# Performance work log

Hardware: AMD Instinct MI355X
Metric: run time of the kernel (lower is better)

Reference implementation:

```python
import jax, jax.numpy as jnp
import numpy as np

D_MODEL = 1024
N_HEADS = 16
D_HEAD = 64
NUM_REL_POS = 2047
B = 8
L = 1024


def setup_inputs() -> dict:
    key = jax.random.key(0)
    ks = jax.random.split(key, 8)
    s = 1.0 / np.sqrt(D_MODEL)
    x = jax.random.normal(ks[0], (B, L, D_MODEL), dtype=jnp.float32)
    rel_indices = jax.random.randint(ks[1], (L, L), 0, NUM_REL_POS)
    Wq = jax.random.normal(ks[2], (D_MODEL, D_MODEL), dtype=jnp.float32) * s
    Wk = jax.random.normal(ks[3], (D_MODEL, D_MODEL), dtype=jnp.float32) * s
    Wv = jax.random.normal(ks[4], (D_MODEL, D_MODEL), dtype=jnp.float32) * s
    Wo = jax.random.normal(ks[5], (D_MODEL, D_MODEL), dtype=jnp.float32) * s
    rel_k = jax.random.normal(ks[6], (NUM_REL_POS, D_HEAD), dtype=jnp.float32) * 0.02
    rel_v = jax.random.normal(ks[7], (NUM_REL_POS, D_HEAD), dtype=jnp.float32) * 0.02
    return {"x": x, "rel_indices": rel_indices, "Wq": Wq, "Wk": Wk,
            "Wv": Wv, "Wo": Wo, "rel_k": rel_k, "rel_v": rel_v}


def reference(x, rel_indices, Wq, Wk, Wv, Wo, rel_k, rel_v):
    Bz, Ls, D = x.shape
    H, dk = N_HEADS, D_HEAD
    scale = 1.0 / np.sqrt(dk)
    # torch Linear: y = x @ W.T, weights are [out, in]
    q = jnp.einsum('bld,ed->ble', x, Wq).reshape(Bz, Ls, H, dk).transpose(0, 2, 1, 3)
    k = jnp.einsum('bld,ed->ble', x, Wk).reshape(Bz, Ls, H, dk).transpose(0, 2, 1, 3)
    v = jnp.einsum('bld,ed->ble', x, Wv).reshape(Bz, Ls, H, dk).transpose(0, 2, 1, 3)
    r_k = rel_k[rel_indices]  # (L, L, dk)
    r_v = rel_v[rel_indices]  # (L, L, dk)
    content = jnp.einsum('bhid,bhjd->bhij', q, k)
    rel = jnp.einsum('bhid,ijd->bhij', q, r_k)
    scores = (content + rel) * scale
    probs = jax.nn.softmax(scores, axis=-1)  # dropout = 0 (eval)
    out = jnp.einsum('bhij,bhjd->bhid', probs, v) + jnp.einsum('bhij,ijd->bhid', probs, r_v)
    out = out.transpose(0, 2, 1, 3).reshape(Bz, Ls, D)
    return jnp.einsum('bld,ed->ble', out, Wo)
```

## Files before the change

kernel.cpp:

```cpp
#include <hip/hip_runtime.h>

#define B_ 8
#define H_ 16
#define L_ 1024
#define DH_ 64
#define DM_ 1024
#define NP_ 2047
#define NP2_ 2048
#define SCALE_ 0.125f

#define PS_ 1032
#define HS_ 260

typedef __attribute__((ext_vector_type(8))) short bf16x8;
typedef __attribute__((ext_vector_type(4))) float f32x4;

__device__ __forceinline__ unsigned short f2bf(float x) {
    union { float f; unsigned int u; } v; v.f = x;
    return (unsigned short)((v.u + 0x7FFFu + ((v.u >> 16) & 1u)) >> 16);
}
__device__ __forceinline__ float bf2f(unsigned short b) {
    union { unsigned int u; float f; } v; v.u = ((unsigned int)b) << 16;
    return v.f;
}

template <int MODE>
__global__ __launch_bounds__(256) void proj_gemm(const float* __restrict__ X,
                                                 const float* __restrict__ W,
                                                 float* __restrict__ Yf,
                                                 unsigned short* __restrict__ Y0,
                                                 unsigned short* __restrict__ Y1)
{
    __shared__ __align__(16) float As[16][132];
    __shared__ __align__(16) float Bs[16][132];
    const int t   = threadIdx.x;
    const int tm  = t & 15;
    const int tn  = t >> 4;
    const int row0 = blockIdx.x * 128;
    const int col0 = blockIdx.y * 128;
    const int lr  = t >> 1;
    const int lc  = (t & 1) * 8;

    float acc[8][8];
#pragma unroll
    for (int i = 0; i < 8; ++i)
#pragma unroll
        for (int j = 0; j < 8; ++j) acc[i][j] = 0.f;

    float4 xa, xb, wa, wb;
    const float* xp = X + (size_t)(row0 + lr) * DM_ + lc;
    const float* wp = W + (size_t)(col0 + lr) * DM_ + lc;
    xa = *(const float4*)(xp);     xb = *(const float4*)(xp + 4);
    wa = *(const float4*)(wp);     wb = *(const float4*)(wp + 4);

    for (int k0 = 0; k0 < DM_; k0 += 16) {
        __syncthreads();
        As[lc + 0][lr] = xa.x; As[lc + 1][lr] = xa.y; As[lc + 2][lr] = xa.z; As[lc + 3][lr] = xa.w;
        As[lc + 4][lr] = xb.x; As[lc + 5][lr] = xb.y; As[lc + 6][lr] = xb.z; As[lc + 7][lr] = xb.w;
        Bs[lc + 0][lr] = wa.x; Bs[lc + 1][lr] = wa.y; Bs[lc + 2][lr] = wa.z; Bs[lc + 3][lr] = wa.w;
        Bs[lc + 4][lr] = wb.x; Bs[lc + 5][lr] = wb.y; Bs[lc + 6][lr] = wb.z; Bs[lc + 7][lr] = wb.w;
        __syncthreads();
        if (k0 + 16 < DM_) {
            xa = *(const float4*)(xp + k0 + 16);  xb = *(const float4*)(xp + k0 + 20);
            wa = *(const float4*)(wp + k0 + 16);  wb = *(const float4*)(wp + k0 + 20);
        }
#pragma unroll
        for (int kk = 0; kk < 16; ++kk) {
            float4 a0 = *(const float4*)&As[kk][tm * 4];
            float4 a1 = *(const float4*)&As[kk][64 + tm * 4];
            float4 b0 = *(const float4*)&Bs[kk][tn * 8];
            float4 b1 = *(const float4*)&Bs[kk][tn * 8 + 4];
            const float av[8] = {a0.x, a0.y, a0.z, a0.w, a1.x, a1.y, a1.z, a1.w};
            const float bv[8] = {b0.x, b0.y, b0.z, b0.w, b1.x, b1.y, b1.z, b1.w};
#pragma unroll
            for (int i = 0; i < 8; ++i)
#pragma unroll
                for (int j = 0; j < 8; ++j)
                    acc[i][j] = fmaf(av[i], bv[j], acc[i][j]);
        }
    }

    const int bidx = row0 >> 10;
    const int hbase = blockIdx.y * 2 + (tn >> 3);
    const int dbase = (tn & 7) * 8;

    if constexpr (MODE == 1) {
#pragma unroll
        for (int i = 0; i < 8; ++i) {
            const int row = row0 + ((i < 4) ? (tm * 4 + i) : (64 + tm * 4 + i - 4));
            *(float4*)(Yf + (size_t)row * DM_ + col0 + tn * 8)     = make_float4(acc[i][0], acc[i][1], acc[i][2], acc[i][3]);
            *(float4*)(Yf + (size_t)row * DM_ + col0 + tn * 8 + 4) = make_float4(acc[i][4], acc[i][5], acc[i][6], acc[i][7]);
        }
    }
    if constexpr (MODE == 0) {
#pragma unroll
        for (int i = 0; i < 8; ++i) {
            const int row = row0 + ((i < 4) ? (tm * 4 + i) : (64 + tm * 4 + i - 4));
            const int l = row & 1023;
            const size_t base = (((size_t)bidx * H_ + hbase) * L_ + l) * DH_ + dbase;
#pragma unroll
            for (int jh = 0; jh < 2; ++jh) {
                ushort4 hi4, lo4;
                unsigned short* hp = (unsigned short*)&hi4;
                unsigned short* lp = (unsigned short*)&lo4;
#pragma unroll
                for (int j = 0; j < 4; ++j) {
                    const float y = acc[i][jh * 4 + j];
                    unsigned short hb = f2bf(y);
                    hp[j] = hb;
                    lp[j] = f2bf(y - bf2f(hb));
                }
                *(ushort4*)(Y0 + base + jh * 4) = hi4;
                *(ushort4*)(Y1 + base + jh * 4) = lo4;
            }
        }
    }
    if constexpr (MODE == 2) {
#pragma unroll
        for (int j = 0; j < 8; ++j) {
            const int d = dbase + j;
            const size_t cb = ((size_t)(bidx * H_ + hbase) * DH_ + d) * L_;
#pragma unroll
            for (int half = 0; half < 2; ++half) {
                const int l0 = (row0 & 1023) + half * 64 + tm * 4;
                ushort4 v4;
                unsigned short* vp = (unsigned short*)&v4;
#pragma unroll
                for (int i = 0; i < 4; ++i) vp[i] = f2bf(acc[half * 4 + i][j]);
                *(ushort4*)(Y0 + cb + l0) = v4;
            }
        }
    }
}

__global__ __launch_bounds__(256) void prep_rel(const float* __restrict__ rk,
                                                const float* __restrict__ rv,
                                                unsigned short* __restrict__ rk_hi,
                                                unsigned short* __restrict__ rv_t)
{
    const int idx = blockIdx.x * 256 + threadIdx.x;
    const int p = idx >> 6;
    const int d = idx & 63;
    float xk = (p < NP_) ? rk[(size_t)p * DH_ + d] : 0.f;
    rk_hi[idx] = f2bf(xk);
    float xv = (p < NP_) ? rv[(size_t)p * DH_ + d] : 0.f;
    rv_t[(size_t)d * NP2_ + p] = f2bf(xv);
}

__global__ __launch_bounds__(512, 4) void shaw_attn_mfma(
    const unsigned short* __restrict__ qh, const unsigned short* __restrict__ ql,
    const unsigned short* __restrict__ kh, const unsigned short* __restrict__ kl,
    const unsigned short* __restrict__ vt, const int* __restrict__ ridx,
    const unsigned short* __restrict__ rkh, const unsigned short* __restrict__ rvt,
    float* __restrict__ out)
{
    __shared__ __align__(16) unsigned char regionA[16 * PS_ * 2];
    __shared__ __align__(16) unsigned char regionB[16 * HS_ * 4];
    __shared__ float pmax[16][8];
    __shared__ float psum[16][8];

    char*           qrel8 = (char*)regionA;
    unsigned short* Pu    = (unsigned short*)regionA;
    float*          hist  = (float*)regionB;
    float*          red   = (float*)regionB;

    const int t    = threadIdx.x;
    const int w    = t >> 6;
    const int lane = t & 63;
    const int mrow = lane & 15;
    const int grp  = lane >> 4;
    const int i0   = blockIdx.x * 16;
    const int h    = blockIdx.y;
    const int b    = blockIdx.z;
    const size_t bh = (size_t)b * H_ + h;

    const unsigned short* qhp = qh + bh * (size_t)(L_ * DH_);
    const unsigned short* qlp = ql + bh * (size_t)(L_ * DH_);
    const unsigned short* khp = kh + bh * (size_t)(L_ * DH_);
    const unsigned short* klp = kl + bh * (size_t)(L_ * DH_);
    const unsigned short* vtp = vt + bh * (size_t)(DH_ * L_);

    bf16x8 qAh[2], qAl[2];
#pragma unroll
    for (int s = 0; s < 2; ++s) {
        const size_t off = (size_t)(i0 + mrow) * DH_ + s * 32 + grp * 8;
        qAh[s] = *(const bf16x8*)(qhp + off);
        qAl[s] = *(const bf16x8*)(qlp + off);
    }

    {
        const unsigned short* rb = rkh + (size_t)(w * 256 + mrow) * DH_ + grp * 8;
#pragma unroll 4
        for (int tt = 0; tt < 16; ++tt) {
            bf16x8 Bh0 = *(const bf16x8*)(rb + tt * 1024);
            bf16x8 Bh1 = *(const bf16x8*)(rb + tt * 1024 + 32);
            f32x4 c = {0.f, 0.f, 0.f, 0.f};
            c = __builtin_amdgcn_mfma_f32_16x16x32_bf16(qAh[0], Bh0, c, 0, 0, 0);
            c = __builtin_amdgcn_mfma_f32_16x16x32_bf16(qAh[1], Bh1, c, 0, 0, 0);
            const int pcol = (w * 16 + tt) * 16 + mrow;
            unsigned int pk = 0;
#pragma unroll
            for (int r = 0; r < 4; ++r) {
                int qi = (int)rintf(c[r] * 128.f);
                qi = qi > 127 ? 127 : (qi < -127 ? -127 : qi);
                pk |= ((unsigned int)(qi & 0xff)) << (8 * r);
            }
            *(unsigned int*)(qrel8 + pcol * 16 + grp * 4) = pk;
        }
    }
    __syncthreads();

    float sc[8][4];
    {
        const unsigned short* kbh = khp + (size_t)(w * 128 + mrow) * DH_ + grp * 8;
        const unsigned short* kbl = klp + (size_t)(w * 128 + mrow) * DH_ + grp * 8;
#pragma unroll 2
        for (int tt = 0; tt < 8; ++tt) {
            bf16x8 Bh0 = *(const bf16x8*)(kbh + tt * 1024);
            bf16x8 Bh1 = *(const bf16x8*)(kbh + tt * 1024 + 32);
            bf16x8 Bl0 = *(const bf16x8*)(kbl + tt * 1024);
            bf16x8 Bl1 = *(const bf16x8*)(kbl + tt * 1024 + 32);
            f32x4 c = {0.f, 0.f, 0.f, 0.f};
            c = __builtin_amdgcn_mfma_f32_16x16x32_bf16(qAh[0], Bh0, c, 0, 0, 0);
            c = __builtin_amdgcn_mfma_f32_16x16x32_bf16(qAh[1], Bh1, c, 0, 0, 0);
            c = __builtin_amdgcn_mfma_f32_16x16x32_bf16(qAh[0], Bl0, c, 0, 0, 0);
            c = __builtin_amdgcn_mfma_f32_16x16x32_bf16(qAh[1], Bl1, c, 0, 0, 0);
            c = __builtin_amdgcn_mfma_f32_16x16x32_bf16(qAl[0], Bh0, c, 0, 0, 0);
            c = __builtin_amdgcn_mfma_f32_16x16x32_bf16(qAl[1], Bh1, c, 0, 0, 0);
#pragma unroll
            for (int r = 0; r < 4; ++r) sc[tt][r] = c[r] * SCALE_;
        }
    }

#pragma unroll
    for (int tt = 0; tt < 8; ++tt) {
        const int jcol = (w * 8 + tt) * 16 + mrow;
#pragma unroll
        for (int r = 0; r < 4; ++r) {
            const int pidx = ridx[(size_t)(i0 + grp * 4 + r) * L_ + jcol];
            sc[tt][r] = fmaf((float)qrel8[pidx * 16 + grp * 4 + r], SCALE_ / 128.f, sc[tt][r]);
        }
    }

    float mx[4];
#pragma unroll
    for (int r = 0; r < 4; ++r) {
        float m = sc[0][r];
#pragma unroll
        for (int tt = 1; tt < 8; ++tt) m = fmaxf(m, sc[tt][r]);
#pragma unroll
        for (int off = 1; off < 16; off <<= 1) m = fmaxf(m, __shfl_xor(m, off));
        mx[r] = m;
    }
    {
        const float wv0 = (mrow == 0) ? mx[0] : (mrow == 1) ? mx[1] : (mrow == 2) ? mx[2] : mx[3];
        if (mrow < 4) pmax[grp * 4 + mrow][w] = wv0;
    }
    __syncthreads();

    float gm[4];
#pragma unroll
    for (int r = 0; r < 4; ++r) {
        const int rr = grp * 4 + r;
        float m = pmax[rr][0];
#pragma unroll
        for (int u = 1; u < 8; ++u) m = fmaxf(m, pmax[rr][u]);
        gm[r] = m;
    }
    float sm[4] = {0.f, 0.f, 0.f, 0.f};
#pragma unroll
    for (int tt = 0; tt < 8; ++tt) {
        const int jcol = (w * 8 + tt) * 16 + mrow;
#pragma unroll
        for (int r = 0; r < 4; ++r) {
            const float e = __expf(sc[tt][r] - gm[r]);
            sm[r] += e;
            Pu[(grp * 4 + r) * PS_ + jcol] = f2bf(e);
        }
    }
#pragma unroll
    for (int r = 0; r < 4; ++r) {
#pragma unroll
        for (int off = 1; off < 16; off <<= 1) sm[r] += __shfl_xor(sm[r], off);
    }
    {
        const float sv0 = (mrow == 0) ? sm[0] : (mrow == 1) ? sm[1] : (mrow == 2) ? sm[2] : sm[3];
        if (mrow < 4) psum[grp * 4 + mrow][w] = sv0;
    }
    __syncthreads();

    const int n = w & 3;
    const int khalf = w >> 2;
    f32x4 acc = {0.f, 0.f, 0.f, 0.f};
    {
        const unsigned short* vcol = vtp + (size_t)(n * 16 + mrow) * L_ + khalf * 512 + grp * 8;
#pragma unroll 4
        for (int s = 0; s < 16; ++s) {
            bf16x8 a  = *(const bf16x8*)(Pu + mrow * PS_ + khalf * 512 + s * 32 + grp * 8);
            bf16x8 bb = *(const bf16x8*)(vcol + s * 32);
            acc = __builtin_amdgcn_mfma_f32_16x16x32_bf16(a, bb, acc, 0, 0, 0);
        }
    }

    for (int pass = 0; pass < 8; ++pass) {
        {
            float4* h4 = (float4*)hist;
            const float4 z4 = make_float4(0.f, 0.f, 0.f, 0.f);
            for (int z = t; z < (16 * HS_) / 4; z += 512) h4[z] = z4;
        }
        __syncthreads();
#pragma unroll
        for (int tt = 0; tt < 8; ++tt) {
            const int jcol = (w * 8 + tt) * 16 + mrow;
#pragma unroll
            for (int r = 0; r < 4; ++r) {
                const int rr = grp * 4 + r;
                const int pidx = ridx[(size_t)(i0 + rr) * L_ + jcol];
                if ((pidx >> 8) == pass)
                    atomicAdd(&hist[rr * HS_ + (pidx & 255)], bf2f(Pu[rr * PS_ + jcol]));
            }
        }
        __syncthreads();
        const unsigned short* rvcol =
            rvt + (size_t)(n * 16 + mrow) * NP2_ + pass * 256 + khalf * 128 + grp * 8;
#pragma unroll
        for (int s = 0; s < 4; ++s) {
            const int kb = khalf * 128 + s * 32;
            const f32x4* hp = (const f32x4*)&hist[mrow * HS_ + kb + grp * 8];
            f32x4 h0 = hp[0], h1 = hp[1];
            bf16x8 a;
#pragma unroll
            for (int e = 0; e < 4; ++e) { a[e] = (short)f2bf(h0[e]); a[e + 4] = (short)f2bf(h1[e]); }
            bf16x8 bb = *(const bf16x8*)(rvcol + s * 32);
            acc = __builtin_amdgcn_mfma_f32_16x16x32_bf16(a, bb, acc, 0, 0, 0);
        }
        __syncthreads();
    }

#pragma unroll
    for (int r = 0; r < 4; ++r) red[w * 320 + (grp * 4 + r) * 20 + mrow] = acc[r];
    __syncthreads();
    if (w < 4) {
#pragma unroll
        for (int r = 0; r < 4; ++r) {
            const int rr = grp * 4 + r;
            float o = red[w * 320 + rr * 20 + mrow] + red[(w + 4) * 320 + rr * 20 + mrow];
            float ssum = 0.f;
#pragma unroll
            for (int u = 0; u < 8; ++u) ssum += psum[rr][u];
            out[((size_t)b * L_ + i0 + rr) * DM_ + h * DH_ + w * 16 + mrow] = o / ssum;
        }
    }
}

extern "C" void kernel_launch(void* const* d_in, const int* in_sizes, int n_in,
                              void* d_out, int out_size, void* d_ws, size_t ws_size,
                              hipStream_t stream)
{
    const float* x    = (const float*)d_in[0];
    const int*   ridx = (const int*)  d_in[1];
    const float* Wq   = (const float*)d_in[2];
    const float* Wk   = (const float*)d_in[3];
    const float* Wv   = (const float*)d_in[4];
    const float* Wo   = (const float*)d_in[5];
    const float* rk   = (const float*)d_in[6];
    const float* rv   = (const float*)d_in[7];
    float* out = (float*)d_out;

    const size_t NQ = (size_t)B_ * H_ * L_ * DH_;
    float* attn = (float*)d_ws;
    unsigned short* u = (unsigned short*)(attn + NQ);
    unsigned short* qh = u;            u += NQ;
    unsigned short* ql = u;            u += NQ;
    unsigned short* kh = u;            u += NQ;
    unsigned short* kl = u;            u += NQ;
    unsigned short* vt = u;            u += NQ;
    unsigned short* rkh = u;           u += (size_t)NP2_ * DH_;
    unsigned short* rvt = u;           u += (size_t)NP2_ * DH_;

    dim3 gthr(256);
    dim3 ggrid((B_ * L_) / 128, DM_ / 128);

    prep_rel<<<dim3((NP2_ * DH_) / 256), gthr, 0, stream>>>(rk, rv, rkh, rvt);
    proj_gemm<0><<<ggrid, gthr, 0, stream>>>(x, Wq, nullptr, qh, ql);
    proj_gemm<0><<<ggrid, gthr, 0, stream>>>(x, Wk, nullptr, kh, kl);
    proj_gemm<2><<<ggrid, gthr, 0, stream>>>(x, Wv, nullptr, vt, nullptr);

    shaw_attn_mfma<<<dim3(L_ / 16, H_, B_), dim3(512), 0, stream>>>(
        qh, ql, kh, kl, vt, ridx, rkh, rvt, attn);

    proj_gemm<1><<<ggrid, gthr, 0, stream>>>(attn, Wo, out, nullptr, nullptr);
}
```

Before: 2.148 ms.

## Deepen projection GEMM K-tile and cache packed rel indices in registers

The fp32 projection GEMM now stages 32 K-elements per shared-memory tile instead of 16, which halves the number of barrier/load rounds per output tile and doubles LDS usage. In the attention kernel, the relative-position indices are packed two per 32-bit register when first read for the score bias. They are then reused across all 8 histogram passes instead of being reloaded from global memory each pass. This adds 16 live registers, which may pressure occupancy.

```diff
diff --git a/kernel.cpp b/kernel.cpp
--- a/kernel.cpp
+++ b/kernel.cpp
@@ -31,15 +31,15 @@
                                                  unsigned short* __restrict__ Y0,
                                                  unsigned short* __restrict__ Y1)
 {
-    __shared__ __align__(16) float As[16][132];
-    __shared__ __align__(16) float Bs[16][132];
+    __shared__ __align__(16) float As[32][132];
+    __shared__ __align__(16) float Bs[32][132];
     const int t   = threadIdx.x;
     const int tm  = t & 15;
     const int tn  = t >> 4;
     const int row0 = blockIdx.x * 128;
     const int col0 = blockIdx.y * 128;
     const int lr  = t >> 1;
-    const int lc  = (t & 1) * 8;
+    const int lc  = (t & 1) * 16;
 
     float acc[8][8];
 #pragma unroll
@@ -47,25 +47,31 @@
 #pragma unroll
         for (int j = 0; j < 8; ++j) acc[i][j] = 0.f;
 
-    float4 xa, xb, wa, wb;
+    float4 xr[4], wr[4];
     const float* xp = X + (size_t)(row0 + lr) * DM_ + lc;
     const float* wp = W + (size_t)(col0 + lr) * DM_ + lc;
-    xa = *(const float4*)(xp);     xb = *(const float4*)(xp + 4);
-    wa = *(const float4*)(wp);     wb = *(const float4*)(wp + 4);
-
-    for (int k0 = 0; k0 < DM_; k0 += 16) {
+#pragma unroll
+    for (int q = 0; q < 4; ++q) { xr[q] = *(const float4*)(xp + q * 4); wr[q] = *(const float4*)(wp + q * 4); }
+
+    for (int k0 = 0; k0 < DM_; k0 += 32) {
         __syncthreads();
-        As[lc + 0][lr] = xa.x; As[lc + 1][lr] = xa.y; As[lc + 2][lr] = xa.z; As[lc + 3][lr] = xa.w;
-        As[lc + 4][lr] = xb.x; As[lc + 5][lr] = xb.y; As[lc + 6][lr] = xb.z; As[lc + 7][lr] = xb.w;
-        Bs[lc + 0][lr] = wa.x; Bs[lc + 1][lr] = wa.y; Bs[lc + 2][lr] = wa.z; Bs[lc + 3][lr] = wa.w;
-        Bs[lc + 4][lr] = wb.x; Bs[lc + 5][lr] = wb.y; Bs[lc + 6][lr] = wb.z; Bs[lc + 7][lr] = wb.w;
+#pragma unroll
+        for (int q = 0; q < 4; ++q) {
+            As[lc + q * 4 + 0][lr] = xr[q].x; As[lc + q * 4 + 1][lr] = xr[q].y;
+            As[lc + q * 4 + 2][lr] = xr[q].z; As[lc + q * 4 + 3][lr] = xr[q].w;
+            Bs[lc + q * 4 + 0][lr] = wr[q].x; Bs[lc + q * 4 + 1][lr] = wr[q].y;
+            Bs[lc + q * 4 + 2][lr] = wr[q].z; Bs[lc + q * 4 + 3][lr] = wr[q].w;
+        }
         __syncthreads();
-        if (k0 + 16 < DM_) {
-            xa = *(const float4*)(xp + k0 + 16);  xb = *(const float4*)(xp + k0 + 20);
-            wa = *(const float4*)(wp + k0 + 16);  wb = *(const float4*)(wp + k0 + 20);
-        }
-#pragma unroll
-        for (int kk = 0; kk < 16; ++kk) {
+        if (k0 + 32 < DM_) {
+#pragma unroll
+            for (int q = 0; q < 4; ++q) {
+                xr[q] = *(const float4*)(xp + k0 + 32 + q * 4);
+                wr[q] = *(const float4*)(wp + k0 + 32 + q * 4);
+            }
+        }
+#pragma unroll
+        for (int kk = 0; kk < 32; ++kk) {
             float4 a0 = *(const float4*)&As[kk][tm * 4];
             float4 a1 = *(const float4*)&As[kk][64 + tm * 4];
             float4 b0 = *(const float4*)&Bs[kk][tn * 8];
@@ -232,14 +238,20 @@
         }
     }
 
+    unsigned int pidxPk[16];
 #pragma unroll
     for (int tt = 0; tt < 8; ++tt) {
         const int jcol = (w * 8 + tt) * 16 + mrow;
+        unsigned int pk0 = 0, pk1 = 0;
 #pragma unroll
         for (int r = 0; r < 4; ++r) {
             const int pidx = ridx[(size_t)(i0 + grp * 4 + r) * L_ + jcol];
             sc[tt][r] = fmaf((float)qrel8[pidx * 16 + grp * 4 + r], SCALE_ / 128.f, sc[tt][r]);
-        }
+            if (r < 2) pk0 |= ((unsigned int)pidx) << (16 * r);
+            else       pk1 |= ((unsigned int)pidx) << (16 * (r - 2));
+        }
+        pidxPk[tt * 2]     = pk0;
+        pidxPk[tt * 2 + 1] = pk1;
     }
 
     float mx[4];
@@ -313,11 +325,16 @@
         for (int tt = 0; tt < 8; ++tt) {
             const int jcol = (w * 8 + tt) * 16 + mrow;
 #pragma unroll
-            for (int r = 0; r < 4; ++r) {
-                const int rr = grp * 4 + r;
-                const int pidx = ridx[(size_t)(i0 + rr) * L_ + jcol];
-                if ((pidx >> 8) == pass)
-                    atomicAdd(&hist[rr * HS_ + (pidx & 255)], bf2f(Pu[rr * PS_ + jcol]));
+            for (int rp = 0; rp < 2; ++rp) {
+                const unsigned int pk = pidxPk[tt * 2 + rp];
+#pragma unroll
+                for (int j = 0; j < 2; ++j) {
+                    const int r  = rp * 2 + j;
+                    const int rr = grp * 4 + r;
+                    const int pidx = (int)((pk >> (16 * j)) & 0xffffu);
+                    if ((pidx >> 8) == pass)
+                        atomicAdd(&hist[rr * HS_ + (pidx & 255)], bf2f(Pu[rr * PS_ + jcol]));
+                }
             }
         }
         __syncthreads();
```

After: 2.165 ms. Within noise of the previous version (+0.8%).
